# Performance work log

Measured on AMD Instinct MI355X. Metric: run time of the kernel, lower is better.

## Reference

```python
import jax, jax.numpy as jnp
import numpy as np

N_HEADS = 16
D_EMBED = 1024
N_CROSS = 768
D_HEAD = D_EMBED // N_HEADS


def setup_inputs() -> dict:
    key = jax.random.key(0)
    ks = jax.random.split(key, 10)
    B, S = 2, 2048
    x = jax.random.normal(ks[0], (B, S, D_EMBED), dtype=jnp.float32)
    context = jax.random.normal(ks[1], (B, S, N_CROSS), dtype=jnp.float32)
    sq = 1.0 / np.sqrt(D_EMBED)
    sc = 1.0 / np.sqrt(N_CROSS)
    Wq = jax.random.normal(ks[2], (D_EMBED, D_EMBED), dtype=jnp.float32) * sq
    bq = jnp.zeros((D_EMBED,), dtype=jnp.float32)
    Wk = jax.random.normal(ks[3], (N_CROSS, D_EMBED), dtype=jnp.float32) * sc
    bk = jnp.zeros((D_EMBED,), dtype=jnp.float32)
    Wv = jax.random.normal(ks[4], (N_CROSS, D_EMBED), dtype=jnp.float32) * sc
    bv = jnp.zeros((D_EMBED,), dtype=jnp.float32)
    Wo = jax.random.normal(ks[5], (D_EMBED, D_EMBED), dtype=jnp.float32) * sq
    bo = jnp.zeros((D_EMBED,), dtype=jnp.float32)
    return {"x": x, "context": context, "Wq": Wq, "bq": bq, "Wk": Wk, "bk": bk,
            "Wv": Wv, "bv": bv, "Wo": Wo, "bo": bo}


def reference(x, context, Wq, bq, Wk, bk, Wv, bv, Wo, bo):
    B, S, _ = x.shape

    def split_heads(t):  # [B,S,E] -> [B,H,S,Dh]
        return t.reshape(B, S, N_HEADS, D_HEAD).transpose(0, 2, 1, 3)

    q = split_heads(x @ Wq + bq)
    k = split_heads(context @ Wk + bk)
    v = split_heads(context @ Wv + bv)

    scale = 1.0 / np.sqrt(D_HEAD)
    scores = jnp.einsum('bhqd,bhkd->bhqk', q, k) * scale
    attn = jax.nn.softmax(scores, axis=-1)
    out = jnp.einsum('bhqk,bhkd->bhqd', attn, v)
    out = out.transpose(0, 2, 1, 3).reshape(B, S, D_EMBED)
    return out @ Wo + bo
```

## Files before the change

### kernel.cpp

```cpp
#include <hip/hip_runtime.h>
#include <math.h>


namespace {

typedef short bfr __attribute__((ext_vector_type(8)));
typedef short s4v __attribute__((ext_vector_type(4)));
typedef unsigned u4v __attribute__((ext_vector_type(4)));
typedef float accf __attribute__((ext_vector_type(16)));

#define MFMA32(a, b, c) __builtin_amdgcn_mfma_f32_32x32x16_bf16(a, b, c, 0, 0, 0)

__device__ inline short f2bf(float f) {
    unsigned u = __float_as_uint(f);
    u += 0x7fffu + ((u >> 16) & 1u);
    return (short)(u >> 16);
}
__device__ inline float bf2f(short s) {
    return __uint_as_float(((unsigned)(unsigned short)s) << 16);
}
__device__ inline float fexp2(float x) { return __builtin_amdgcn_exp2f(x); }
__device__ inline accf zero16() {
    accf z;
#pragma unroll
    for (int i = 0; i < 16; ++i) z[i] = 0.f;
    return z;
}
__device__ inline void dma16(const void* g, void* l) {
    __builtin_amdgcn_global_load_lds(
        (const __attribute__((address_space(1))) void*)g,
        (__attribute__((address_space(3))) void*)l, 16, 0, 0);
}

__global__ __launch_bounds__(256) void prep(
    const float* __restrict__ x, const float* __restrict__ ctx,
    short* __restrict__ xb, short* __restrict__ cb,
    const float* __restrict__ Wq, const float* __restrict__ Wk,
    const float* __restrict__ Wv, const float* __restrict__ Wo,
    short* __restrict__ Wqt, short* __restrict__ Wkt,
    short* __restrict__ Wvt, short* __restrict__ Wot) {
    __shared__ short t[64][68];
    const int bx = blockIdx.x;
    if (bx < 7168) {
        int i = bx * 256 + threadIdx.x;
        if (i < 1048576) {
            float4 v = ((const float4*)x)[i];
            s4v p = {f2bf(v.x), f2bf(v.y), f2bf(v.z), f2bf(v.w)};
            ((s4v*)xb)[i] = p;
        } else {
            int j = i - 1048576;
            float4 v = ((const float4*)ctx)[j];
            s4v p = {f2bf(v.x), f2bf(v.y), f2bf(v.z), f2bf(v.w)};
            ((s4v*)cb)[j] = p;
        }
        return;
    }
    const int idx = bx - 7168;
    const int z = idx >> 8, gy = (idx >> 4) & 15, gx = idx & 15;
    const float* W;
    short* Wt;
    int K;
    switch (z) {
        case 0: W = Wq; Wt = Wqt; K = 1024; break;
        case 1: W = Wk; Wt = Wkt; K = 768; break;
        case 2: W = Wv; Wt = Wvt; K = 768; break;
        default: W = Wo; Wt = Wot; K = 1024; break;
    }
    const int k0 = gy * 64;
    if (k0 >= K) return;
    const int tid = threadIdx.x;
    const int n0 = gx * 64;
    const int kr = tid >> 4, nc = (tid & 15) * 4;
#pragma unroll
    for (int rep = 0; rep < 4; ++rep) {
        int k = kr + rep * 16;
        float4 v = *(const float4*)&W[(size_t)(k0 + k) * 1024 + n0 + nc];
        t[nc + 0][k] = f2bf(v.x);
        t[nc + 1][k] = f2bf(v.y);
        t[nc + 2][k] = f2bf(v.z);
        t[nc + 3][k] = f2bf(v.w);
    }
    __syncthreads();
    const int nr = tid >> 4, kc = (tid & 15) * 4;
#pragma unroll
    for (int rep = 0; rep < 4; ++rep) {
        int n = nr + rep * 16;
        s4v p = {t[n][kc], t[n][kc + 1], t[n][kc + 2], t[n][kc + 3]};
        *(s4v*)&Wt[(size_t)(n0 + n) * K + k0 + kc] = p;
    }
}

__global__ __launch_bounds__(256) void gemm_qkv(
    const short* __restrict__ xb, const short* __restrict__ cb,
    const short* __restrict__ Wqt, const short* __restrict__ Wkt,
    const short* __restrict__ Wvt, const float* __restrict__ bq,
    const float* __restrict__ bk, const float* __restrict__ bv,
    short* __restrict__ Qf, short* __restrict__ Kf, short* __restrict__ Vt,
    float qscale) {
    const int bid = blockIdx.x;
    const int z = bid >> 8;
    const int local = bid & 255;
    const short* A  = (z == 0) ? xb : cb;
    const short* Bt = (z == 0) ? Wqt : ((z == 1) ? Wkt : Wvt);
    const float* bias = (z == 0) ? bq : ((z == 1) ? bk : bv);
    const int K = (z == 0) ? 1024 : 768;
    const int NIT = K / 32;
    const float scale = (z == 0) ? qscale : 1.f;
    short* out = (z == 0) ? Qf : ((z == 1) ? Kf : Vt);

    __shared__ short As[8192];
    __shared__ short Bs[8192];
    const int t = threadIdx.x, lane = t & 63, w = t >> 6;
    const int lm = lane & 31, h2 = lane >> 5;
    const int wm = w & 1, wn = w >> 1;
    const int m0 = (local & 31) * 128, n0 = (local >> 5) * 128;

    const int st = t ^ ((t >> 3) & 7);
    const int srow = st >> 2, scol = (st & 3) * 8;
    const short* ga = A + (size_t)(m0 + srow) * K + scol;
    const short* gb = Bt + (size_t)(n0 + srow) * K + scol;

    const int xorv = (lm >> 1) & 7;
    const int rA0 = wm * 64 + lm, rB0 = wn * 64 + lm;

    accf acc[2][2] = {zero16(), zero16(), zero16(), zero16()};

    dma16(ga, &As[w * 512]);
    dma16(ga + (size_t)64 * K, &As[2048 + w * 512]);
    dma16(gb, &Bs[w * 512]);
    dma16(gb + (size_t)64 * K, &Bs[2048 + w * 512]);

#pragma unroll 1
    for (int it = 0; it < NIT; ++it) {
        const int p = it & 1;
        __syncthreads();
        if (it + 1 < NIT) {
            const int kt = (it + 1) * 32;
            short* lA = &As[(1 - p) * 4096 + w * 512];
            short* lB = &Bs[(1 - p) * 4096 + w * 512];
            dma16(ga + kt, lA);
            dma16(ga + (size_t)64 * K + kt, lA + 2048);
            dma16(gb + kt, lB);
            dma16(gb + (size_t)64 * K + kt, lB + 2048);
        }
        const short* bA = &As[p * 4096];
        const short* bB = &Bs[p * 4096];
#pragma unroll
        for (int kk8 = 0; kk8 < 4; kk8 += 2) {
            bfr a0 = *(const bfr*)&bA[((rA0 * 4 + h2 + kk8) ^ xorv) * 8];
            bfr a1 = *(const bfr*)&bA[(((rA0 + 32) * 4 + h2 + kk8) ^ xorv) * 8];
            bfr b0 = *(const bfr*)&bB[((rB0 * 4 + h2 + kk8) ^ xorv) * 8];
            bfr b1 = *(const bfr*)&bB[(((rB0 + 32) * 4 + h2 + kk8) ^ xorv) * 8];
            acc[0][0] = MFMA32(a0, b0, acc[0][0]);
            acc[0][1] = MFMA32(a0, b1, acc[0][1]);
            acc[1][0] = MFMA32(a1, b0, acc[1][0]);
            acc[1][1] = MFMA32(a1, b1, acc[1][1]);
        }
    }

#pragma unroll
    for (int nt = 0; nt < 2; ++nt) {
        const int n = n0 + wn * 64 + nt * 32 + lm;
        const float bn = bias[n];
        const int hh = n >> 6, dd = n & 63;
#pragma unroll
        for (int mt = 0; mt < 2; ++mt) {
            const int mbase = m0 + wm * 64 + mt * 32 + 4 * h2;
            if (z != 2) {
                const int cb2 = (dd >> 4) * 512 + ((dd >> 3) & 1) * 256 + (dd & 7);
#pragma unroll
                for (int r = 0; r < 16; ++r) {
                    const int m = mbase + (r & 3) + 8 * (r >> 2);
                    const int bb = m >> 11, q = m & 2047;
                    float v = (acc[mt][nt][r] + bn) * scale;
                    out[((size_t)((bb * 16 + hh) * 64 + (q >> 5))) * 2048 +
                        cb2 + (q & 31) * 8] = f2bf(v);
                }
            } else {
                const int dblk = dd >> 5, lmv = dd & 31;
#pragma unroll
                for (int g = 0; g < 4; ++g) {
                    const int m = mbase + 8 * g;
                    const int bb = m >> 11, s = m & 2047;
                    const int kvt = s >> 6, kc = (s >> 4) & 3;
                    const int h2v = (s >> 3) & 1, j0 = s & 7;
                    s4v p = {f2bf(acc[mt][nt][4 * g + 0] + bn),
                             f2bf(acc[mt][nt][4 * g + 1] + bn),
                             f2bf(acc[mt][nt][4 * g + 2] + bn),
                             f2bf(acc[mt][nt][4 * g + 3] + bn)};
                    *(s4v*)(out +
                            ((size_t)(((bb * 16 + hh) * 32 + kvt) * 2 + dblk)) * 2048 +
                            kc * 512 + h2v * 256 + lmv * 8 + j0) = p;
                }
            }
        }
    }
}

__global__ __launch_bounds__(512) void gemm_out(
    const short* __restrict__ p0, const short* __restrict__ p1,
    const float* __restrict__ lsum, const short* __restrict__ Bt,
    const float* __restrict__ bias, float* __restrict__ out) {
    constexpr int K = 1024, NIT = 32;
    __shared__ short As[8192];
    __shared__ short Bs[8192];
    const int t = threadIdx.x, lane = t & 63, w = t >> 6;
    const int lm = lane & 31, h2 = lane >> 5;
    const int wm = w & 1, wn = w >> 1;
    const int bid = blockIdx.x;
    const int m0 = (bid & 31) * 128, n0 = (bid >> 5) * 128;

    const int st = t ^ ((t >> 3) & 7);
    const int srow = st >> 2, scol = (st & 3) * 8;
    const int gm = m0 + srow;
    const int b = gm >> 11, q = gm & 2047;
    const short* pa0 = p0 + (size_t)gm * 1024 + scol;
    const short* pa1 = p1 + (size_t)gm * 1024 + scol;
    const short* gb = Bt + (size_t)(n0 + srow) * K + scol;

    float inv[16];
#pragma unroll
    for (int h = 0; h < 16; ++h) {
        float l0 = lsum[((size_t)b * 16 + h) * 2048 + q];
        float l1 = lsum[((size_t)(2 + b) * 16 + h) * 2048 + q];
        inv[h] = 1.f / (l0 + l1);
    }

    const int xorv = (lm >> 1) & 7;
    const int rA0 = wm * 64 + lm, rB0 = wn * 32 + lm;

    accf acc[2] = {zero16(), zero16()};

    dma16(gb, &Bs[w * 512]);
    {
        bfr v0 = *(const bfr*)pa0;
        bfr v1 = *(const bfr*)pa1;
        const float iv = inv[0];
        bfr pk;
#pragma unroll
        for (int j = 0; j < 8; ++j)
            pk[j] = f2bf((bf2f(v0[j]) + bf2f(v1[j])) * iv);
        *(bfr*)&As[t * 8] = pk;
    }

#pragma unroll 1
    for (int it = 0; it < NIT; ++it) {
        const int p = it & 1;
        __syncthreads();
        bfr v0, v1;
        const bool nxt = (it + 1 < NIT);
        if (nxt) {
            const int ktn = (it + 1) * 32;
            dma16(gb + ktn, &Bs[(1 - p) * 4096 + w * 512]);
            v0 = *(const bfr*)(pa0 + ktn);
            v1 = *(const bfr*)(pa1 + ktn);
        }
        const short* bA = &As[p * 4096];
        const short* bB = &Bs[p * 4096];
#pragma unroll
        for (int kk8 = 0; kk8 < 4; kk8 += 2) {
            bfr a0 = *(const bfr*)&bA[((rA0 * 4 + h2 + kk8) ^ xorv) * 8];
            bfr a1 = *(const bfr*)&bA[(((rA0 + 32) * 4 + h2 + kk8) ^ xorv) * 8];
            bfr b0 = *(const bfr*)&bB[((rB0 * 4 + h2 + kk8) ^ xorv) * 8];
            acc[0] = MFMA32(a0, b0, acc[0]);
            acc[1] = MFMA32(a1, b0, acc[1]);
        }
        if (nxt) {
            const float iv = inv[(it + 1) >> 1];
            bfr pk;
#pragma unroll
            for (int j = 0; j < 8; ++j)
                pk[j] = f2bf((bf2f(v0[j]) + bf2f(v1[j])) * iv);
            *(bfr*)&As[(1 - p) * 4096 + t * 8] = pk;
        }
    }

    const int n = n0 + wn * 32 + lm;
    const float bn = bias[n];
#pragma unroll
    for (int mt = 0; mt < 2; ++mt) {
        const int mbase = m0 + wm * 64 + mt * 32 + 4 * h2;
#pragma unroll
        for (int r = 0; r < 16; ++r) {
            const int m = mbase + (r & 3) + 8 * (r >> 2);
            out[(size_t)m * 1024 + n] = acc[mt][r] + bn;
        }
    }
}

__global__ __launch_bounds__(256, 3) void attn(
    const short* __restrict__ Qf, const short* __restrict__ Kf,
    const short* __restrict__ Vt, short* __restrict__ part,
    float* __restrict__ lsum) {
    __shared__ short smem[16384];
    const int bid = blockIdx.x;
    const int hidx = bid & 31, qs = bid >> 5;
    const int split = qs & 1, qb = qs >> 1;
    const int b = hidx >> 4, h = hidx & 15;
    const int lane = threadIdx.x & 63, wv = threadIdx.x >> 6;
    const int lm = lane & 31, h2 = lane >> 5;
    const bool hb = h2 != 0;
    const int q0 = qb * 128 + wv * 32;

    const short* qbase =
        Qf + ((size_t)(hidx * 64 + (q0 >> 5))) * 2048 + lane * 8;
    bfr qf[4];
#pragma unroll
    for (int kc = 0; kc < 4; ++kc) qf[kc] = *(const bfr*)(qbase + kc * 512);

    const short* khead = Kf + (size_t)hidx * 131072 + split * 65536;
    const short* vhead = Vt + (size_t)hidx * 131072 + split * 65536;
    const short* gsrc =
        ((wv < 2) ? (khead + wv * 2048) : (vhead + (wv - 2) * 2048)) + lane * 8;

#pragma unroll
    for (int i = 0; i < 4; ++i)
        dma16(gsrc + i * 512, &smem[wv * 2048 + i * 512]);

    accf oa0 = zero16(), oa1 = zero16();
    float la0 = 0.f, la1 = 0.f;

#pragma unroll 1
    for (int it = 0; it < 16; ++it) {
        const int p = it & 1;
        __syncthreads();
        if (it + 1 < 16) {
            const short* gn = gsrc + (size_t)(it + 1) * 4096;
            short* ln = &smem[(1 - p) * 8192 + wv * 2048];
#pragma unroll
            for (int i = 0; i < 4; ++i) dma16(gn + i * 512, ln + i * 512);
        }
        const short* kb = &smem[p * 8192];
        bfr kf0[4], kf1[4], vf0[4], vf1[4];
#pragma unroll
        for (int kc = 0; kc < 4; ++kc) {
            kf0[kc] = *(const bfr*)&kb[kc * 512 + lane * 8];
            kf1[kc] = *(const bfr*)&kb[2048 + kc * 512 + lane * 8];
            vf0[kc] = *(const bfr*)&kb[4096 + kc * 512 + lane * 8];
            vf1[kc] = *(const bfr*)&kb[6144 + kc * 512 + lane * 8];
        }
        accf s0 = zero16(), s1 = zero16();
#pragma unroll
        for (int kc = 0; kc < 4; ++kc) {
            s0 = MFMA32(kf0[kc], qf[kc], s0);
            s1 = MFMA32(kf1[kc], qf[kc], s1);
        }

#pragma unroll
        for (int i = 0; i < 16; ++i) s0[i] = fexp2(s0[i]);
#pragma unroll
        for (int i = 0; i < 16; ++i) s1[i] = fexp2(s1[i]);
#pragma unroll
        for (int i = 0; i < 16; ++i) {
            if (i & 1) la1 += s0[i] + s1[i];
            else       la0 += s0[i] + s1[i];
        }

        bfr pb[4];
#pragma unroll
        for (int kc = 0; kc < 4; ++kc) {
            const accf& s = (kc < 2) ? s0 : s1;
            const int base = 8 * (kc & 1);
            unsigned Lw0 = __builtin_amdgcn_perm(__float_as_uint(s[base + 1]),
                                                 __float_as_uint(s[base + 0]),
                                                 0x07060302u);
            unsigned Lw1 = __builtin_amdgcn_perm(__float_as_uint(s[base + 3]),
                                                 __float_as_uint(s[base + 2]),
                                                 0x07060302u);
            unsigned Hw0 = __builtin_amdgcn_perm(__float_as_uint(s[base + 5]),
                                                 __float_as_uint(s[base + 4]),
                                                 0x07060302u);
            unsigned Hw1 = __builtin_amdgcn_perm(__float_as_uint(s[base + 7]),
                                                 __float_as_uint(s[base + 6]),
                                                 0x07060302u);
            unsigned c0 = hb ? Lw0 : Hw0;
            unsigned c1 = hb ? Lw1 : Hw1;
            unsigned r0 = (unsigned)__shfl_xor((int)c0, 32);
            unsigned r1 = (unsigned)__shfl_xor((int)c1, 32);
            u4v pw = {hb ? r0 : Lw0, hb ? r1 : Lw1,
                      hb ? Hw0 : r0, hb ? Hw1 : r1};
            pb[kc] = __builtin_bit_cast(bfr, pw);
        }

#pragma unroll
        for (int kc = 0; kc < 4; ++kc) {
            oa0 = MFMA32(vf0[kc], pb[kc], oa0);
            oa1 = MFMA32(vf1[kc], pb[kc], oa1);
        }
    }

    float ls = la0 + la1;
    ls += __shfl_xor(ls, 32);
    if (!hb) lsum[((size_t)(split * 2 + b) * 16 + h) * 2048 + q0 + lm] = ls;

    short* orow = part + (size_t)split * 4194304 +
                  (size_t)(b * 2048 + q0 + lm) * 1024 + h * 64;
#pragma unroll
    for (int dt = 0; dt < 2; ++dt) {
        const accf& oa = dt ? oa1 : oa0;
#pragma unroll
        for (int g = 0; g < 4; ++g) {
            const int d0 = dt * 32 + 4 * h2 + 8 * g;
            s4v p = {f2bf(oa[4 * g + 0]), f2bf(oa[4 * g + 1]),
                     f2bf(oa[4 * g + 2]), f2bf(oa[4 * g + 3])};
            *(s4v*)(orow + d0) = p;
        }
    }
}

}

extern "C" void kernel_launch(void* const* d_in, const int* in_sizes, int n_in,
                              void* d_out, int out_size, void* d_ws,
                              size_t ws_size, hipStream_t stream) {
    const float* x   = (const float*)d_in[0];
    const float* ctx = (const float*)d_in[1];
    const float* Wq  = (const float*)d_in[2];
    const float* bq  = (const float*)d_in[3];
    const float* Wk  = (const float*)d_in[4];
    const float* bk  = (const float*)d_in[5];
    const float* Wv  = (const float*)d_in[6];
    const float* bv  = (const float*)d_in[7];
    const float* Wo  = (const float*)d_in[8];
    const float* bo  = (const float*)d_in[9];

    short* xb  = (short*)d_ws;
    short* cb  = xb + (size_t)4096 * 1024;
    short* Wqt = cb + (size_t)4096 * 768;
    short* Wkt = Wqt + (size_t)1024 * 1024;
    short* Wvt = Wkt + (size_t)1024 * 768;
    short* Wot = Wvt + (size_t)1024 * 768;
    short* Qf  = Wot + (size_t)1024 * 1024;
    short* Kf  = Qf + (size_t)4096 * 1024;
    short* Vt  = Kf + (size_t)4096 * 1024;
    short* p0  = Vt + (size_t)4096 * 1024;
    short* p1  = p0 + (size_t)4096 * 1024;
    float* lsum = (float*)(p1 + (size_t)4096 * 1024);

    prep<<<8192, 256, 0, stream>>>(x, ctx, xb, cb, Wq, Wk, Wv, Wo,
                                   Wqt, Wkt, Wvt, Wot);

    const float qscale = 0.125f * 1.44269504088896f;
    gemm_qkv<<<768, 256, 0, stream>>>(xb, cb, Wqt, Wkt, Wvt,
                                      bq, bk, bv, Qf, Kf, Vt, qscale);

    attn<<<1024, 256, 0, stream>>>(Qf, Kf, Vt, p0, lsum);

    gemm_out<<<256, 512, 0, stream>>>(p0, p1, lsum, Wot, bo, (float*)d_out);
}
```

Baseline: 216.9 us.

## Use 4-stage smem ring with 32-key tiles and counted vmcnt waits in attention

Restructures the attention main loop to process 32-key tiles over 32 iterations with a 4-slot shared-memory ring buffer. Loads are prefetched three tiles ahead, and an explicit vmcnt(4) wait replaces the full sync-based double buffer. The aim is to hide global-to-LDS DMA latency better and to reduce register pressure per iteration. The cost is twice as many barriers and smaller MFMA batches per iteration. The loop also issues wrapped-around extra prefetches at the end, which are drained with vmcnt(0).

Measured after the change: 216.4 us. No clear change (-0.2%).

```diff
diff --git a/kernel.cpp b/kernel.cpp
--- a/kernel.cpp
+++ b/kernel.cpp
@@ -310,68 +310,75 @@
 
     const short* khead = Kf + (size_t)hidx * 131072 + split * 65536;
     const short* vhead = Vt + (size_t)hidx * 131072 + split * 65536;
-    const short* gsrc =
-        ((wv < 2) ? (khead + wv * 2048) : (vhead + (wv - 2) * 2048)) + lane * 8;
-
-#pragma unroll
-    for (int i = 0; i < 4; ++i)
-        dma16(gsrc + i * 512, &smem[wv * 2048 + i * 512]);
+
+    const short* gbase = ((wv < 2) ? (khead + wv * 1024)
+                                   : (vhead + (wv - 2) * 2048)) + lane * 8;
+    const int ldst = wv * 1024;
+    const bool kwave = (wv < 2);
+
+#pragma unroll
+    for (int pit = 0; pit < 3; ++pit) {
+        const int go = kwave ? pit * 2048
+                             : ((pit >> 1) * 4096 + (pit & 1) * 1024);
+        dma16(gbase + go, &smem[pit * 4096 + ldst]);
+        dma16(gbase + go + 512, &smem[pit * 4096 + ldst + 512]);
+        __builtin_amdgcn_sched_barrier(0);
+    }
 
     accf oa0 = zero16(), oa1 = zero16();
     float la0 = 0.f, la1 = 0.f;
 
 #pragma unroll 1
-    for (int it = 0; it < 16; ++it) {
-        const int p = it & 1;
-        __syncthreads();
-        if (it + 1 < 16) {
-            const short* gn = gsrc + (size_t)(it + 1) * 4096;
-            short* ln = &smem[(1 - p) * 8192 + wv * 2048];
-#pragma unroll
-            for (int i = 0; i < 4; ++i) dma16(gn + i * 512, ln + i * 512);
-        }
-        const short* kb = &smem[p * 8192];
-        bfr kf0[4], kf1[4], vf0[4], vf1[4];
-#pragma unroll
-        for (int kc = 0; kc < 4; ++kc) {
-            kf0[kc] = *(const bfr*)&kb[kc * 512 + lane * 8];
-            kf1[kc] = *(const bfr*)&kb[2048 + kc * 512 + lane * 8];
-            vf0[kc] = *(const bfr*)&kb[4096 + kc * 512 + lane * 8];
-            vf1[kc] = *(const bfr*)&kb[6144 + kc * 512 + lane * 8];
-        }
-        accf s0 = zero16(), s1 = zero16();
-#pragma unroll
-        for (int kc = 0; kc < 4; ++kc) {
-            s0 = MFMA32(kf0[kc], qf[kc], s0);
-            s1 = MFMA32(kf1[kc], qf[kc], s1);
-        }
+    for (int it = 0; it < 32; ++it) {
+        __builtin_amdgcn_sched_barrier(0);
+        asm volatile("s_waitcnt vmcnt(4)" ::: "memory");
+        __builtin_amdgcn_s_barrier();
+        __builtin_amdgcn_sched_barrier(0);
+        {
+            const int nx = (it + 3) & 31;
+            const int go = kwave ? nx * 2048
+                                 : ((nx >> 1) * 4096 + (nx & 1) * 1024);
+            short* l = &smem[((it + 3) & 3) * 4096 + ldst];
+            dma16(gbase + go, l);
+            dma16(gbase + go + 512, l + 512);
+        }
+        const short* kb = &smem[(it & 3) * 4096];
+        bfr kf[4], vf0[2], vf1[2];
+#pragma unroll
+        for (int kc = 0; kc < 4; ++kc)
+            kf[kc] = *(const bfr*)&kb[kc * 512 + lane * 8];
+#pragma unroll
+        for (int kc = 0; kc < 2; ++kc) {
+            vf0[kc] = *(const bfr*)&kb[2048 + kc * 512 + lane * 8];
+            vf1[kc] = *(const bfr*)&kb[3072 + kc * 512 + lane * 8];
+        }
+        accf s0 = zero16();
+#pragma unroll
+        for (int kc = 0; kc < 4; ++kc) s0 = MFMA32(kf[kc], qf[kc], s0);
 
 #pragma unroll
         for (int i = 0; i < 16; ++i) s0[i] = fexp2(s0[i]);
 #pragma unroll
-        for (int i = 0; i < 16; ++i) s1[i] = fexp2(s1[i]);
-#pragma unroll
         for (int i = 0; i < 16; ++i) {
-            if (i & 1) la1 += s0[i] + s1[i];
-            else       la0 += s0[i] + s1[i];
-        }
-
-        bfr pb[4];
-#pragma unroll
-        for (int kc = 0; kc < 4; ++kc) {
-            const accf& s = (kc < 2) ? s0 : s1;
-            const int base = 8 * (kc & 1);
-            unsigned Lw0 = __builtin_amdgcn_perm(__float_as_uint(s[base + 1]),
-                                                 __float_as_uint(s[base + 0]),
+            if (i & 1) la1 += s0[i];
+            else       la0 += s0[i];
+        }
+
+        bfr pb[2];
+#pragma unroll
+        for (int kc = 0; kc < 2; ++kc) {
+            const int base = 8 * kc;
+            unsigned Lw0 = __builtin_amdgcn_perm(__float_as_uint(s0[base + 1]),
+                                                 __float_as_uint(s0[base + 0]),
                                                  0x07060302u);
-            unsigned Lw1 = __builtin_amdgcn_perm(__float_as_uint(s[base + 3]),
-                                                 __float_as_uint(s[base + 2]),
+            unsigned Lw1 = __builtin_amdgcn_perm(__float_as_uint(s0[base + 3]),
+                                                 __float_as_uint(s0[base + 2]),
                                                  0x07060302u);
-            unsigned Hw0 = __builtin_amdgcn_perm(__float_as_uint(s[base + 5]),
-                                                 __float_as_uint(s[base + 4]),
+            unsigned Hw0 = __builtin_amdgcn_perm(__float_as_uint(s0[base + 5]),
+                                                 __float_as_uint(s0[base + 4]),
                                                  0x07060302u);
-            unsigned Hw1 = __builtin_amdgcn_perm(__float_as_uint(s[base + 7]),
-                                                 __float_as_uint(s[base + 6]),
+            unsigned Hw1 = __builtin_amdgcn_perm(__float_as_uint(s0[base + 7]),
+                                                 __float_as_uint(s0[base + 6]),
                                                  0x07060302u);
             unsigned c0 = hb ? Lw0 : Hw0;
             unsigned c1 = hb ? Lw1 : Hw1;
@@ -383,11 +390,14 @@
         }
 
 #pragma unroll
-        for (int kc = 0; kc < 4; ++kc) {
+        for (int kc = 0; kc < 2; ++kc) {
             oa0 = MFMA32(vf0[kc], pb[kc], oa0);
             oa1 = MFMA32(vf1[kc], pb[kc], oa1);
         }
     }
+
+    asm volatile("s_waitcnt vmcnt(0)" ::: "memory");
+    __builtin_amdgcn_sched_barrier(0);
 
     float ls = la0 + la1;
     ls += __shfl_xor(ls, 32);
```
